# Performance work log

Hardware: AMD Instinct MI355X
Metric: run time of the kernel (lower is better)

The kernel has to match this reference:

```python
import jax, jax.numpy as jnp
import numpy as np

T, B, S, V = 50, 64, 400, 50000
D = 512; E = 512; H = 512; A = 512; POOL = 2


def setup_inputs() -> dict:
    key = jax.random.key(0)
    ks = jax.random.split(key, 20)
    def rn(k, shape, s=0.05):
        return jax.random.normal(k, shape, jnp.float32) * s
    return {
        "input_y": jax.random.randint(ks[0], (T, B), 0, V),
        "hidden": rn(ks[1], (1, B, H), 1.0),
        "context": rn(ks[2], (S, B, E), 1.0),
        "src_pad_mask": jnp.zeros((B, S), jnp.float32),
        "init_att": rn(ks[3], (B, E), 1.0),
        "coverage": jnp.zeros((B, S), jnp.float32),
        "global_ctx": rn(ks[4], (B, E), 1.0),
        "emb_W": rn(ks[5], (V, D)).at[0].set(0.0),  # padding_idx=0
        "W_ih": rn(ks[6], (3 * H, D + E)),
        "W_hh": rn(ks[7], (3 * H, H)),
        "b_ih": jnp.zeros((3 * H,), jnp.float32),
        "b_hh": jnp.zeros((3 * H,), jnp.float32),
        "W_pre": rn(ks[8], (E, A)),
        "b_pre": jnp.zeros((A,), jnp.float32),
        "W_q": rn(ks[9], (H + E, A)),
        "W_v": rn(ks[10], (A,)),
        "W_cov": rn(ks[11], (A,)),
        "W_pgen": rn(ks[12], (E + H + D,)),
        "b_pgen": jnp.zeros((), jnp.float32),
        "W_ro": rn(ks[13], (D + H + E + E, H)),
        "b_ro": jnp.zeros((H,), jnp.float32),
    }


def _gru_cell(x, h, W_ih, W_hh, b_ih, b_hh):
    # PyTorch GRUCell gate order: r, z, n
    gi = x @ W_ih.T + b_ih
    gh = h @ W_hh.T + b_hh
    i_r, i_z, i_n = jnp.split(gi, 3, axis=-1)
    h_r, h_z, h_n = jnp.split(gh, 3, axis=-1)
    r = jax.nn.sigmoid(i_r + h_r)
    z = jax.nn.sigmoid(i_z + h_z)
    n = jnp.tanh(i_n + r * h_n)
    return (1.0 - z) * n + z * h


def reference(input_y, hidden, context, src_pad_mask, init_att, coverage, global_ctx,
              emb_W, W_ih, W_hh, b_ih, b_hh, W_pre, b_pre, W_q, W_v, W_cov,
              W_pgen, b_pgen, W_ro, b_ro):
    emb = emb_W[input_y]                      # [T,B,D]
    ctx = jnp.transpose(context, (1, 0, 2))   # [B,S,E]
    precompute = ctx @ W_pre + b_pre          # [B,S,A] (computed once, as in module)
    pad = src_pad_mask > 0.5
    NEG = jnp.float32(-1e18)

    def step(carry, emb_t):
        h, cur_ctx, cov = carry
        x = jnp.concatenate([emb_t, cur_ctx], 1)          # input feed
        h0 = _gru_cell(x, h[0], W_ih, W_hh, b_ih, b_hh)   # layers=1
        h = h.at[0].set(h0)
        output = h0
        # concat attention with coverage
        q = jnp.concatenate([output, global_ctx], 1) @ W_q          # [B,A]
        tmp = jnp.tanh(precompute + q[:, None, :] + cov[..., None] * W_cov)
        energy = tmp @ W_v                                           # [B,S]
        energy = jnp.where(pad, NEG, energy)
        attn = jax.nn.softmax(energy, axis=1)
        cur_ctx = jnp.einsum('bs,bse->be', attn, ctx)
        # pointer-gen
        p_gen = jax.nn.sigmoid(
            jnp.concatenate([cur_ctx, output, emb_t], 1) @ W_pgen + b_pgen)[:, None]
        # readout + maxout (dropout is identity in eval)
        readout = jnp.concatenate([emb_t, output, cur_ctx, global_ctx], 1) @ W_ro + b_ro
        mo = readout.reshape(B, H // POOL, POOL).max(axis=-1)        # [B,H/POOL]
        cov_loss = jnp.sum(jnp.minimum(attn, cov), 1)                # cov_loss_wt=1.0
        next_cov = cov + attn
        return (h, cur_ctx, next_cov), (mo, p_gen, attn, cov_loss)

    (hidden_f, cur_ctx_f, cov_f), (g_out, g_pg, g_attn, cov_losses) = jax.lax.scan(
        step, (hidden, init_att, coverage), emb)
    return (g_out, hidden_f, g_attn[-1], cur_ctx_f, g_pg, g_attn, cov_losses, cov_f)
```

## Files before the change

### kernel.cpp

```cpp
#include <hip/hip_runtime.h>
#include <hip/hip_bf16.h>


#define T_STEPS 50
#define BB 64
#define SS 400

#define O_GOUT 0
#define O_HID 819200
#define O_ATTN_LAST 851968
#define O_CTXF 877568
#define O_PG 910336
#define O_GATTN 913536
#define O_COVL 2193536
#define O_COVF 2196736

typedef __attribute__((ext_vector_type(4))) float f4;
typedef __attribute__((ext_vector_type(8))) short s8v;
typedef __attribute__((ext_vector_type(4))) unsigned u4;

static __device__ __forceinline__ float bf2f(unsigned short u){
  unsigned v = ((unsigned)u) << 16; return __builtin_bit_cast(float, v);
}
static __device__ __forceinline__ unsigned short f2bf(float f){
  unsigned u = __builtin_bit_cast(unsigned, f);
  unsigned r = (u + 0x7FFFu + ((u >> 16) & 1u)) >> 16;
  return (unsigned short)r;
}
static __device__ __forceinline__ float sigmoidf_(float x){ return 1.f/(1.f+__expf(-x)); }
static __device__ __forceinline__ float tanhf_(float x){ float e=__expf(2.f*x); return 1.f - 2.f/(e+1.f); }
static __device__ __forceinline__ float ald32f(const float* p){
  unsigned u = __hip_atomic_load((const unsigned*)p, __ATOMIC_RELAXED, __HIP_MEMORY_SCOPE_AGENT);
  return __builtin_bit_cast(float, u);
}
static __device__ __forceinline__ void ast32f(float* p, float v){
  __hip_atomic_store((unsigned*)p, __builtin_bit_cast(unsigned, v),
                     __ATOMIC_RELAXED, __HIP_MEMORY_SCOPE_AGENT);
}

__global__ void conv_ctx(const float* __restrict__ ctx, unsigned short* __restrict__ out){
  int o = blockIdx.x*256 + threadIdx.x;
  if(o >= SS*BB*512) return;
  int e = o & 511; int b = (o>>9)&63; int s = o>>15;
  out[((b*SS+s)<<9) + e] = f2bf(ctx[o]);
}
__global__ void conv_emb(const int* __restrict__ y, const float* __restrict__ embW,
                         unsigned short* __restrict__ embU){
  int o = blockIdx.x*256+threadIdx.x; if(o>=T_STEPS*BB*512) return;
  int d = o & 511; int i = o>>9;
  embU[o] = f2bf(embW[(long)y[i]*512 + d]);
}
__global__ void conv_rest(const float* __restrict__ W_ih, const float* __restrict__ W_hh,
                          const float* __restrict__ W_pre, const float* __restrict__ W_ro,
                          const float* __restrict__ W_q,
                          const float* __restrict__ hidden, const float* __restrict__ init_att,
                          const float* __restrict__ gctx, const float* __restrict__ coverage,
                          unsigned short* __restrict__ wihbf, unsigned short* __restrict__ wpreT,
                          unsigned short* __restrict__ wroT, unsigned short* __restrict__ Wgru,
                          unsigned short* __restrict__ WqP,
                          float* __restrict__ hrow0, unsigned short* __restrict__ h0bf_init,
                          unsigned short* __restrict__ ctx0bf, float* __restrict__ gctxT,
                          float* __restrict__ cov, unsigned* __restrict__ flags){
  int o = blockIdx.x*256+threadIdx.x;
  if(o < 786432){
    int j = o>>9; int d = o&511;
    wihbf[o] = f2bf(W_ih[(long)j*1024 + d]);
  } else if(o < 1048576){
    int p = o - 786432;
    int a = p>>9; int e = p&511;
    wpreT[p] = f2bf(W_pre[(long)e*512 + a]);
  } else if(o < 2097152){
    int p = o - 1048576;
    int n = p>>11; int k = p&2047;
    wroT[p] = f2bf(W_ro[(long)k*512 + n]);
  } else if(o < 3670016){
    int p = o - 2097152;
    int rg = p >> 13; int rem = p & 8191;
    int ki = rem >> 9; int ln = (rem >> 3) & 63; int e = p & 7;
    int blk = rg/24; int r2 = rg%24; int w = r2/6; int r3 = r2%6; int g = r3>>1; int op = r3&1;
    int rl = ln & 15; int kk = ((ln>>4)<<3) + e;
    int d = blk*64 + w*16 + rl; int j = g*512 + d; int k = ki*32 + kk;
    float v = op ? W_hh[(long)j*512 + k] : W_ih[(long)j*1024 + 512 + k];
    Wgru[p] = f2bf(v);
  } else if(o < 3932160){
    int p = o - 3670016;
    int e = p&7; int ln=(p>>3)&63; int kf=(p>>9)&1; int nrg=(p>>10)&31; int blk=p>>15;
    int n = nrg*16 + (ln&15);
    int k = blk*64 + kf*32 + ((ln>>4)<<3) + e;
    WqP[p] = f2bf(W_q[(long)k*512 + n]);
  } else if(o < 4056128){
    int p = o - 3932160;
    if(p < 32768){ float v = hidden[p]; hrow0[p] = v; h0bf_init[p] = f2bf(v); }
    else if(p < 65536){ int q=p-32768; ctx0bf[q] = f2bf(init_att[q]); }
    else if(p < 98304){ int q=p-65536; int b=q>>9,e=q&511; gctxT[e*64+b]=gctx[q]; }
    else if(p < 123904){ int q=p-98304; cov[q]=coverage[q]; }
    else { int q=p-123904; if(q<64) flags[q]=0u; }
  }
}

template<int OUT_BF16>
__global__ __launch_bounds__(256) void mfma_gemm(
    const unsigned short* __restrict__ Abf, int lda,
    const unsigned short* __restrict__ Bbf, int ldb,
    void* __restrict__ Cp, int ldc, const float* __restrict__ bias, int K)
{
  __shared__ __align__(16) unsigned short Ash[128*40];
  __shared__ __align__(16) unsigned short Bsh[128*40];
  int m0 = blockIdx.x*128, n0 = blockIdx.y*128;
  int tid = threadIdx.x;
  int wid = tid>>6, lane = tid&63;
  int wm = wid>>1, wn = wid&1;
  int lr = lane&15, lg = lane>>4;
  f4 acc[4][4];
  #pragma unroll
  for(int i=0;i<4;i++)
    #pragma unroll
    for(int j=0;j<4;j++) acc[i][j]=(f4)0.f;

  for(int kt=0; kt<K; kt+=32){
    #pragma unroll
    for(int c=0;c<2;c++){
      int flat = tid*16 + c*8;
      int row = flat>>5, col = flat&31;
      const unsigned short* ga = Abf + (long)(m0+row)*lda + kt + col;
      *(uint4*)(&Ash[row*40+col]) = *(const uint4*)ga;
      const unsigned short* gb = Bbf + (long)(n0+row)*ldb + kt + col;
      *(uint4*)(&Bsh[row*40+col]) = *(const uint4*)gb;
    }
    __syncthreads();
    s8v av[4], bv[4];
    #pragma unroll
    for(int mi=0;mi<4;mi++) av[mi] = *(const s8v*)(&Ash[(wm*64+mi*16+lr)*40 + lg*8]);
    #pragma unroll
    for(int ni=0;ni<4;ni++) bv[ni] = *(const s8v*)(&Bsh[(wn*64+ni*16+lr)*40 + lg*8]);
    #pragma unroll
    for(int mi=0;mi<4;mi++)
      #pragma unroll
      for(int ni=0;ni<4;ni++)
        acc[mi][ni] = __builtin_amdgcn_mfma_f32_16x16x32_bf16(av[mi], bv[ni], acc[mi][ni], 0,0,0);
    __syncthreads();
  }
  #pragma unroll
  for(int mi=0;mi<4;mi++)
    #pragma unroll
    for(int ni=0;ni<4;ni++){
      int gc = n0 + wn*64 + ni*16 + lr;
      #pragma unroll
      for(int r=0;r<4;r++){
        int gr = m0 + wm*64 + mi*16 + lg*4 + r;
        float v = acc[mi][ni][r];
        if(bias) v += bias[gc];
        if(OUT_BF16) ((unsigned short*)Cp)[(long)gr*ldc + gc] = f2bf(v);
        else         ((float*)Cp)[(long)gr*ldc + gc] = v;
      }
    }
}

__global__ __launch_bounds__(256) void mfma_gemm_ro(
    const unsigned short* __restrict__ embU, const unsigned short* __restrict__ h0bf,
    const unsigned short* __restrict__ ctxA, const unsigned short* __restrict__ wroT,
    float* __restrict__ RO, const float* __restrict__ bias)
{
  __shared__ __align__(16) unsigned short Ash[128*40];
  __shared__ __align__(16) unsigned short Bsh[128*40];
  int m0 = blockIdx.x*128, n0 = blockIdx.y*128;
  int tid = threadIdx.x;
  int wid = tid>>6, lane = tid&63;
  int wm = wid>>1, wn = wid&1;
  int lr = lane&15, lg = lane>>4;
  f4 acc[4][4];
  #pragma unroll
  for(int i=0;i<4;i++)
    #pragma unroll
    for(int j=0;j<4;j++) acc[i][j]=(f4)0.f;

  for(int kt=0; kt<1536; kt+=32){
    const unsigned short* src = (kt<512) ? embU : (kt<1024) ? h0bf : ctxA;
    int klocal = kt & 511;
    #pragma unroll
    for(int c=0;c<2;c++){
      int flat = tid*16 + c*8;
      int row = flat>>5, col = flat&31;
      *(uint4*)(&Ash[row*40+col]) = *(const uint4*)(src + (long)(m0+row)*512 + klocal + col);
      *(uint4*)(&Bsh[row*40+col]) = *(const uint4*)(wroT + (long)(n0+row)*2048 + kt + col);
    }
    __syncthreads();
    s8v av[4], bv[4];
    #pragma unroll
    for(int mi=0;mi<4;mi++) av[mi] = *(const s8v*)(&Ash[(wm*64+mi*16+lr)*40 + lg*8]);
    #pragma unroll
    for(int ni=0;ni<4;ni++) bv[ni] = *(const s8v*)(&Bsh[(wn*64+ni*16+lr)*40 + lg*8]);
    #pragma unroll
    for(int mi=0;mi<4;mi++)
      #pragma unroll
      for(int ni=0;ni<4;ni++)
        acc[mi][ni] = __builtin_amdgcn_mfma_f32_16x16x32_bf16(av[mi], bv[ni], acc[mi][ni], 0,0,0);
    __syncthreads();
  }
  #pragma unroll
  for(int mi=0;mi<4;mi++)
    #pragma unroll
    for(int ni=0;ni<4;ni++){
      int gc = n0 + wn*64 + ni*16 + lr;
      #pragma unroll
      for(int r=0;r<4;r++){
        int gr = m0 + wm*64 + mi*16 + lg*4 + r;
        RO[(long)gr*512 + gc] = acc[mi][ni][r] + bias[gc];
      }
    }
}

__global__ __launch_bounds__(256) void small2(
  const float* __restrict__ AT, const float* __restrict__ W_q, const float* __restrict__ W_ro,
  float* __restrict__ q_g, float* __restrict__ ro_g)
{
  int blk = blockIdx.x;
  int half = blk>>7; int nblk = blk&127;
  int tid = threadIdx.x;
  int b = tid&63; int nq = tid>>6;
  int n = __builtin_amdgcn_readfirstlane(nblk*4 + nq);
  const float* W = half ? W_ro : W_q;
  int koff = half ? 1536 : 512;
  float acc = 0.f;
  const float* wp = W + (long)koff*512 + n;
  #pragma unroll 8
  for(int k=0;k<512;k++){
    acc = fmaf(AT[k*64+b], wp[(long)k*512], acc);
  }
  (half ? ro_g : q_g)[b*512+n] = acc;
}

__global__ __launch_bounds__(512) void k_step(
  const unsigned short* __restrict__ ctx0bf, float* __restrict__ ctxP,
  float* __restrict__ S_part, float* __restrict__ P_exp,
  const unsigned short* __restrict__ hprevbf,
  const float* __restrict__ hrow_in, float* __restrict__ hrow_out,
  const unsigned short* __restrict__ Wp, const unsigned short* __restrict__ WqP,
  const float* __restrict__ gi_emb, const float* __restrict__ b_hh,
  unsigned short* __restrict__ h0bf_all, float* __restrict__ qpart,
  float* __restrict__ cov, unsigned short* __restrict__ ctxA,
  const unsigned short* __restrict__ pre, const unsigned short* __restrict__ ctxbf,
  const float* __restrict__ q_g, const float* __restrict__ Wv,
  const float* __restrict__ Wcov, const float* __restrict__ padm,
  float* __restrict__ covl_part, unsigned* __restrict__ flags,
  float* __restrict__ outp, int t)
{
  __shared__ __align__(16) char smem[75008];
  const int blk = blockIdx.x;
  const int tid = threadIdx.x;
  const int w = tid>>6, lane = tid&63;
  const int lr = lane&15, lg = lane>>4;

  if(blk < 8){
    unsigned short* Ash = (unsigned short*)smem;
    unsigned short* HS  = (unsigned short*)(smem+65536);
    float* invS = (float*)(smem+74752);
    const int swz = (lr&7)<<4;
    const int dg = w&3, bh = w>>2;
    const int rgbase = blk*24 + dg*6;

    if(t>0 && tid<64){
      const float* Sp = S_part + ((t-1)&1)*256 + tid*4;
      invS[tid] = 1.f/(Sp[0]+Sp[1]+Sp[2]+Sp[3]);
    }
    __syncthreads();

    f4 acc2[6][2];
    #pragma unroll
    for(int u=0;u<6;u++)
      #pragma unroll
      for(int mm=0;mm<2;mm++) acc2[u][mm]=(f4)0.f;

    for(int kp=0; kp<2; kp++){
      for(int c = tid; c < 4096; c += 512){
        int op = c>>11; int row = (c>>5)&63; int kc = c&31;
        int e0 = kp*256 + kc*8;
        u4 v;
        if(op){
          v = *(const u4*)(hprevbf + row*512 + e0);
        } else if(t>0){
          const float* cp = ctxP + (long)row*2048 + e0;
          float sc = invS[row];
          f4 a0 = *(const f4*)(cp);
          f4 a1 = *(const f4*)(cp+512);
          f4 a2 = *(const f4*)(cp+1024);
          f4 a3 = *(const f4*)(cp+1536);
          f4 b0 = *(const f4*)(cp+4);
          f4 b1 = *(const f4*)(cp+516);
          f4 b2 = *(const f4*)(cp+1028);
          f4 b3 = *(const f4*)(cp+1540);
          f4 s0 = (a0+a1+a2+a3)*sc;
          f4 s1 = (b0+b1+b2+b3)*sc;
          v.x = (unsigned)f2bf(s0.x) | ((unsigned)f2bf(s0.y)<<16);
          v.y = (unsigned)f2bf(s0.z) | ((unsigned)f2bf(s0.w)<<16);
          v.z = (unsigned)f2bf(s1.x) | ((unsigned)f2bf(s1.y)<<16);
          v.w = (unsigned)f2bf(s1.z) | ((unsigned)f2bf(s1.w)<<16);
          if(blk == (row>>3))
            *(u4*)(ctxA + ((long)((t-1)*64+row))*512 + e0) = v;
        } else {
          v = *(const u4*)(ctx0bf + row*512 + e0);
        }
        int dst = op*32768 + row*512 + ((kc*16) ^ ((row&7)<<4));
        *(u4*)((char*)Ash + dst) = v;
      }
      __syncthreads();
      {
        #pragma unroll 2
        for(int ktl=0; ktl<256; ktl+=32){
          s8v av[2][2];
          #pragma unroll
          for(int op=0;op<2;op++)
            #pragma unroll
            for(int mm=0;mm<2;mm++){
              int mi = bh*2+mm;
              av[op][mm] = *(const s8v*)((const char*)Ash + op*32768 + (mi*16+lr)*512 + ((ktl*2 + lg*16) ^ swz));
            }
          int ki = kp*8 + (ktl>>5);
          const unsigned short* wb = Wp + (long)rgbase*8192 + ki*512 + lane*8;
          #pragma unroll
          for(int u=0;u<6;u++){
            s8v bv = *(const s8v*)(wb + (long)u*8192);
            #pragma unroll
            for(int mm=0;mm<2;mm++)
              acc2[u][mm] = __builtin_amdgcn_mfma_f32_16x16x32_bf16(av[u&1][mm], bv, acc2[u][mm], 0,0,0);
          }
        }
      }
      __syncthreads();
    }

    {
      int d = blk*64 + dg*16 + lr;
      float bhr = b_hh[d], bhz = b_hh[512+d], bhn = b_hh[1024+d];
      #pragma unroll
      for(int mm=0;mm<2;mm++){
        int mi = bh*2+mm;
        #pragma unroll
        for(int r=0;r<4;r++){
          int b = mi*16 + lg*4 + r;
          const float* ge = gi_emb + (long)(t*64+b)*1536;
          float g0 = __builtin_nontemporal_load(ge + d);
          float g1 = __builtin_nontemporal_load(ge + 512 + d);
          float g2 = __builtin_nontemporal_load(ge + 1024 + d);
          float rr = sigmoidf_(g0 + bhr + acc2[0][mm][r] + acc2[1][mm][r]);
          float zz = sigmoidf_(g1 + bhz + acc2[2][mm][r] + acc2[3][mm][r]);
          float nn = tanhf_(  g2       + acc2[4][mm][r] + rr*(acc2[5][mm][r] + bhn));
          float hp = hrow_in[b*512 + d];
          float hv = (1.f-zz)*nn + zz*hp;
          hrow_out[b*512+d] = hv;
          unsigned short hb = f2bf(hv);
          h0bf_all[(long)(t*64+b)*512 + d] = hb;
          HS[b*72 + dg*16 + lr] = hb;
          if(t==T_STEPS-1) outp[O_HID + b*512 + d] = hv;
        }
      }
    }
    __syncthreads();
    {
      #pragma unroll
      for(int i=0;i<8;i++){
        f4 accq[2];
        accq[0]=(f4)0.f; accq[1]=(f4)0.f;
        #pragma unroll
        for(int kf=0;kf<2;kf++){
          s8v bv = *(const s8v*)(WqP + ((((long)blk*32 + (dg*8+i))*2 + kf)*64 + lane)*8);
          #pragma unroll
          for(int mm=0;mm<2;mm++){
            int mi = bh*2+mm;
            s8v av = *(const s8v*)(HS + (mi*16+lr)*72 + kf*32 + lg*8);
            accq[mm] = __builtin_amdgcn_mfma_f32_16x16x32_bf16(av, bv, accq[mm], 0,0,0);
          }
        }
        int n = dg*128 + i*16 + lr;
        #pragma unroll
        for(int mm=0;mm<2;mm++)
          #pragma unroll
          for(int r=0;r<4;r++)
            ast32f(qpart + (long)blk*32768 + (long)((bh*2+mm)*16+lg*4+r)*512 + n, accq[mm][r]);
      }
    }
    asm volatile("s_waitcnt vmcnt(0)" ::: "memory");
    __syncthreads();
    if(tid==0)
      __hip_atomic_fetch_add(flags+t, 1u, __ATOMIC_RELEASE, __HIP_MEMORY_SCOPE_AGENT);
    return;
  }

  {
    int eb = blk-8; int b = eb>>2, cq = eb&3, c0 = cq*100;
    float* q_sh  = (float*)smem;
    float* wv_sh = (float*)(smem+2048);
    float* wc_sh = (float*)(smem+4096);
    float* covL  = (float*)(smem+6144);
    float* padL  = (float*)(smem+6560);
    float* red   = (float*)(smem+7392);
    float* red2  = (float*)(smem+9440);
    float* pb    = (float*)(smem+9472);

    wv_sh[tid]=Wv[tid]; wc_sh[tid]=Wcov[tid];
    if(tid<100) padL[tid]=padm[b*400+c0+tid];
    float clp = 0.f;
    if(t>0){
      const float* Sp = S_part + ((t-1)&1)*256 + b*4;
      float inv = 1.f/(Sp[0]+Sp[1]+Sp[2]+Sp[3]);
      if(tid<100){
        float p = P_exp[b*400+c0+tid]*inv;
        float co = cov[b*400+c0+tid];
        clp = fminf(p,co);
        float nc = co+p;
        cov[b*400+c0+tid]=nc;
        covL[tid]=nc;
        outp[O_GATTN + (long)(t-1)*25600 + b*400 + c0 + tid] = p;
      }
    } else {
      if(tid<100) covL[tid]=cov[b*400+c0+tid];
    }
    const unsigned short* prow = pre   + (((long)(b*400+c0))<<9) + lane*8;
    const unsigned short* crow = ctxbf + (((long)(b*400+c0))<<9) + lane*8;
    u4 pr[13], cr[13];
    #pragma unroll
    for(int j=0;j<13;j++){
      int i = w + j*8;
      long ro = (long)((i<100)? i : 0) << 9;
      pr[j] = *(const u4*)(prow + ro);
      cr[j] = *(const u4*)(crow + ro);
    }
    red[tid]=clp; __syncthreads();
    for(int o=256;o;o>>=1){ if(tid<o) red[tid]+=red[tid+o]; __syncthreads(); }
    if(t>0 && tid==0) covl_part[(long)(t-1)*256 + b*4+cq] = red[0];
    if(tid==0){
      unsigned it=0;
      while(__hip_atomic_load(flags+t, __ATOMIC_RELAXED, __HIP_MEMORY_SCOPE_AGENT) < 8u){
        __builtin_amdgcn_s_sleep(8);
        if(++it > 200000000u) break;
      }
    }
    __syncthreads();
    asm volatile("" ::: "memory");
    {
      float acc = q_g[b*512+tid];
      #pragma unroll
      for(int p=0;p<8;p++) acc += ald32f(qpart + ((long)p<<15) + b*512 + tid);
      q_sh[tid] = acc;
    }
    __syncthreads();
    float wsum = 0.f;
    float acc8[8];
    #pragma unroll
    for(int j=0;j<8;j++) acc8[j]=0.f;
    #pragma unroll
    for(int j=0;j<13;j++){
      int i = w + j*8;
      if(i<100){
        u4 cur = pr[j];
        const unsigned* uu = (const unsigned*)&cur;
        float cv = covL[i];
        float part = 0.f;
        #pragma unroll
        for(int q4=0;q4<4;q4++){
          int a = lane*8 + q4*2;
          part += wv_sh[a]  * tanhf_(bf2f((unsigned short)(uu[q4]&0xffffu)) + q_sh[a]   + cv*wc_sh[a]);
          part += wv_sh[a+1]* tanhf_(bf2f((unsigned short)(uu[q4]>>16))    + q_sh[a+1] + cv*wc_sh[a+1]);
        }
        #pragma unroll
        for(int off=32;off;off>>=1) part += __shfl_xor(part, off, 64);
        float e = (padL[i]>0.5f) ? -1e18f : part;
        float p = __expf(e);
        if(lane==0) P_exp[b*400+c0+i] = p;
        wsum += p;
        u4 cc = cr[j];
        const unsigned* cu = (const unsigned*)&cc;
        acc8[0] = fmaf(p, bf2f((unsigned short)(cu[0]&0xffffu)), acc8[0]);
        acc8[1] = fmaf(p, bf2f((unsigned short)(cu[0]>>16)),     acc8[1]);
        acc8[2] = fmaf(p, bf2f((unsigned short)(cu[1]&0xffffu)), acc8[2]);
        acc8[3] = fmaf(p, bf2f((unsigned short)(cu[1]>>16)),     acc8[3]);
        acc8[4] = fmaf(p, bf2f((unsigned short)(cu[2]&0xffffu)), acc8[4]);
        acc8[5] = fmaf(p, bf2f((unsigned short)(cu[2]>>16)),     acc8[5]);
        acc8[6] = fmaf(p, bf2f((unsigned short)(cu[3]&0xffffu)), acc8[6]);
        acc8[7] = fmaf(p, bf2f((unsigned short)(cu[3]>>16)),     acc8[7]);
      }
    }
    if(lane==0) red2[w]=wsum;
    __syncthreads();
    if(tid==0)
      S_part[(t&1)*256 + b*4+cq] = red2[0]+red2[1]+red2[2]+red2[3]+red2[4]+red2[5]+red2[6]+red2[7];
    #pragma unroll
    for(int j=0;j<8;j++) pb[w*512 + lane*8+j] = acc8[j];
    __syncthreads();
    {
      float v = pb[tid]+pb[512+tid]+pb[1024+tid]+pb[1536+tid]
               +pb[2048+tid]+pb[2560+tid]+pb[3072+tid]+pb[3584+tid];
      ctxP[((long)b*4+cq)*512 + tid] = v;
    }
  }
}

__global__ __launch_bounds__(256) void k_fin(
  const float* __restrict__ ctxP, const float* __restrict__ S_part,
  const float* __restrict__ P_exp, const float* __restrict__ cov,
  const float* __restrict__ covl_part,
  unsigned short* __restrict__ ctxA, float* __restrict__ outp)
{
  __shared__ float red[256];
  int b = blockIdx.x; int tid = threadIdx.x;
  const int tb = T_STEPS-1;
  const float* Sp = S_part + 256 + b*4;
  float S = Sp[0]+Sp[1]+Sp[2]+Sp[3];
  float inv = 1.f/S;
  float clp;
  {
    float p = P_exp[b*400+tid]*inv;
    float co = cov[b*400+tid];
    clp = fminf(p, co);
    float nc = co+p;
    outp[O_GATTN + (long)tb*25600 + b*400 + tid] = p;
    outp[O_ATTN_LAST + b*400 + tid] = p;
    outp[O_COVF + b*400 + tid] = nc;
  }
  if(tid<144){
    int i = 256+tid;
    float p = P_exp[b*400+i]*inv;
    float co = cov[b*400+i];
    clp += fminf(p, co);
    float nc = co+p;
    outp[O_GATTN + (long)tb*25600 + b*400 + i] = p;
    outp[O_ATTN_LAST + b*400 + i] = p;
    outp[O_COVF + b*400 + i] = nc;
  }
  red[tid]=clp; __syncthreads();
  for(int o=128;o;o>>=1){ if(tid<o) red[tid]+=red[tid+o]; __syncthreads(); }
  if(tid==0) outp[O_COVL + tb*64 + b] = red[0];
  if(tid<49){
    const float* cp = covl_part + (long)tid*256 + b*4;
    outp[O_COVL + tid*64 + b] = cp[0]+cp[1]+cp[2]+cp[3];
  }
  for(int c=tid;c<512;c+=256){
    float v = (ctxP[(long)b*2048+c]+ctxP[(long)b*2048+512+c]
              +ctxP[(long)b*2048+1024+c]+ctxP[(long)b*2048+1536+c])*inv;
    outp[O_CTXF + b*512 + c] = v;
    ctxA[(long)(tb*64+b)*512 + c] = f2bf(v);
  }
}

__global__ __launch_bounds__(256) void k_post(
  const unsigned short* __restrict__ embU, const unsigned short* __restrict__ h0bf,
  const unsigned short* __restrict__ ctxA, const float* __restrict__ Wpg,
  const float* __restrict__ bpg, const float* __restrict__ RO,
  const float* __restrict__ ro_g, float* __restrict__ outp)
{
  int blk = blockIdx.x;
  if(blk < 800){
    int wid = threadIdx.x>>6, lane=threadIdx.x&63;
    int m = blk*4 + wid;
    float acc=0.f;
    #pragma unroll
    for(int i=0;i<8;i++){
      int k = i*64+lane;
      acc = fmaf(bf2f(ctxA[(long)m*512+k]), Wpg[k], acc);
      acc = fmaf(bf2f(h0bf[(long)m*512+k]), Wpg[512+k], acc);
      acc = fmaf(bf2f(embU[(long)m*512+k]), Wpg[1024+k], acc);
    }
    #pragma unroll
    for(int off=32; off; off>>=1) acc += __shfl_xor(acc, off, 64);
    if(lane==0) outp[O_PG + m] = sigmoidf_(acc + bpg[0]);
  } else {
    int o = (blk-800)*256 + threadIdx.x;
    int h = o & 255; int m = o>>8; int b = m & 63;
    float v0 = RO[(long)m*512 + 2*h]   + ro_g[b*512 + 2*h];
    float v1 = RO[(long)m*512 + 2*h+1] + ro_g[b*512 + 2*h+1];
    outp[O_GOUT + o] = fmaxf(v0,v1);
  }
}

extern "C" void kernel_launch(void* const* d_in, const int* in_sizes, int n_in,
                              void* d_out, int out_size, void* d_ws, size_t ws_size,
                              hipStream_t stream)
{
  (void)in_sizes; (void)n_in; (void)out_size; (void)ws_size;
  const int*   y       = (const int*)d_in[0];
  const float* hidden  = (const float*)d_in[1];
  const float* context = (const float*)d_in[2];
  const float* padm    = (const float*)d_in[3];
  const float* init_att= (const float*)d_in[4];
  const float* coverage= (const float*)d_in[5];
  const float* gctx    = (const float*)d_in[6];
  const float* embW    = (const float*)d_in[7];
  const float* W_ih    = (const float*)d_in[8];
  const float* W_hh    = (const float*)d_in[9];
  const float* b_ih    = (const float*)d_in[10];
  const float* b_hh    = (const float*)d_in[11];
  const float* W_pre   = (const float*)d_in[12];
  const float* b_pre   = (const float*)d_in[13];
  const float* W_q     = (const float*)d_in[14];
  const float* W_v     = (const float*)d_in[15];
  const float* W_cov   = (const float*)d_in[16];
  const float* W_pg    = (const float*)d_in[17];
  const float* b_pg    = (const float*)d_in[18];
  const float* W_ro    = (const float*)d_in[19];
  const float* b_ro    = (const float*)d_in[20];
  float* out = (float*)d_out;

  char* wsb = (char*)d_ws;
  size_t off = 0;
  auto alloc = [&](size_t bytes)->char*{ char* p = wsb+off; off += (bytes+255)&~255UL; return p; };
  unsigned short* pre    = (unsigned short*)alloc(25600UL*512*2);
  unsigned short* ctxbf  = (unsigned short*)alloc(13107200UL*2);
  unsigned short* embU   = (unsigned short*)alloc(3200UL*512*2);
  unsigned short* wihbf  = (unsigned short*)alloc(1536UL*512*2);
  unsigned short* wpreT  = (unsigned short*)alloc(512UL*512*2);
  unsigned short* wroT   = (unsigned short*)alloc(512UL*2048*2);
  unsigned short* Wgru   = (unsigned short*)alloc(192UL*8192*2);
  unsigned short* WqP    = (unsigned short*)alloc(262144UL*2);
  float* gi_emb = (float*)alloc(3200UL*1536*4);
  float* RO     = (float*)alloc(3200UL*512*4);
  float* q_g    = (float*)alloc(64UL*512*4);
  float* ro_g   = (float*)alloc(64UL*512*4);
  float* hrow0  = (float*)alloc(64UL*512*4);
  float* hrow1  = (float*)alloc(64UL*512*4);
  float* gctxT  = (float*)alloc(512UL*64*4);
  unsigned short* h0bf = (unsigned short*)alloc(3200UL*512*2);
  unsigned short* h0bf_init = (unsigned short*)alloc(64UL*512*2);
  unsigned short* ctx0bf    = (unsigned short*)alloc(64UL*512*2);
  unsigned short* ctxA = (unsigned short*)alloc(3200UL*512*2);
  float* ctxP   = (float*)alloc(64UL*4*512*4);
  float* P_exp  = (float*)alloc(64UL*400*4);
  float* S_part = (float*)alloc(2UL*256*4);
  float* qpart  = (float*)alloc(8UL*64*512*4);
  float* cov    = (float*)alloc(64UL*400*4);
  float* covl_part = (float*)alloc(50UL*256*4);
  unsigned* flags = (unsigned*)alloc(64UL*4);

  conv_ctx <<<dim3(51200),dim3(256),0,stream>>>(context, ctxbf);
  conv_emb <<<dim3(6400), dim3(256),0,stream>>>(y, embW, embU);
  conv_rest<<<dim3(15845),dim3(256),0,stream>>>(W_ih, W_hh, W_pre, W_ro, W_q,
                                                hidden, init_att, gctx, coverage,
                                                wihbf, wpreT, wroT, Wgru, WqP,
                                                hrow0, h0bf_init, ctx0bf, gctxT, cov, flags);

  mfma_gemm<1><<<dim3(200,4),dim3(256),0,stream>>>(ctxbf,512, wpreT,512,  pre,   512, b_pre, 512);
  mfma_gemm<0><<<dim3(25,12),dim3(256),0,stream>>>(embU, 512, wihbf,512,  gi_emb,1536, b_ih, 512);
  small2<<<dim3(256),dim3(256),0,stream>>>(gctxT, W_q, W_ro, q_g, ro_g);

  for(int t=0; t<T_STEPS; t++){
    float* hin  = (t&1) ? hrow1 : hrow0;
    float* hout = (t&1) ? hrow0 : hrow1;
    const unsigned short* hprevbf = t ? (h0bf + (long)(t-1)*32768) : h0bf_init;
    k_step<<<dim3(264),dim3(512),0,stream>>>(ctx0bf, ctxP, S_part, P_exp, hprevbf,
                                             hin, hout, Wgru, WqP, gi_emb, b_hh,
                                             h0bf, qpart, cov, ctxA, pre, ctxbf,
                                             q_g, W_v, W_cov, padm, covl_part,
                                             flags, out, t);
  }

  k_fin<<<dim3(64),dim3(256),0,stream>>>(ctxP, S_part, P_exp, cov, covl_part, ctxA, out);
  mfma_gemm_ro<<<dim3(25,4),dim3(256),0,stream>>>(embU, h0bf, ctxA, wroT, RO, b_ro);
  k_post<<<dim3(4000),dim3(256),0,stream>>>(embU, h0bf, ctxA, W_pg, b_pg, RO, ro_g, out);
}
```

Before: 2.779 ms.

## Fuse per-step launches into one persistent cooperative scan kernel with flag sync

Replaces the 50 per-timestep k_step launches with one cooperative persistent kernel of 256 blocks that loops over time. GRU and attention blocks hand off through per-step atomic flags instead of kernel boundaries. The hidden state stays in registers, coverage stays in LDS, the attention block's own finalize runs in-kernel, and qpart is double-buffered. This removes launch overhead and the grid-wide barriers between steps. The cost is spin-wait latency and the correctness risk of a bounded spin loop that can break out early.

```diff
diff --git a/kernel.cpp b/kernel.cpp
--- a/kernel.cpp
+++ b/kernel.cpp
@@ -18,6 +18,7 @@
 typedef __attribute__((ext_vector_type(4))) float f4;
 typedef __attribute__((ext_vector_type(8))) short s8v;
 typedef __attribute__((ext_vector_type(4))) unsigned u4;
+typedef unsigned long long u64;
 
 static __device__ __forceinline__ float bf2f(unsigned short u){
   unsigned v = ((unsigned)u) << 16; return __builtin_bit_cast(float, v);
@@ -37,6 +38,14 @@
   __hip_atomic_store((unsigned*)p, __builtin_bit_cast(unsigned, v),
                      __ATOMIC_RELAXED, __HIP_MEMORY_SCOPE_AGENT);
 }
+static __device__ __forceinline__ u64 ald64(const void* p){
+  return __hip_atomic_load((const u64*)p, __ATOMIC_RELAXED, __HIP_MEMORY_SCOPE_AGENT);
+}
+static __device__ __forceinline__ void ast64(void* p, u64 v){
+  __hip_atomic_store((u64*)p, v, __ATOMIC_RELAXED, __HIP_MEMORY_SCOPE_AGENT);
+}
+static __device__ __forceinline__ float flo(u64 x){ return __builtin_bit_cast(float,(unsigned)x); }
+static __device__ __forceinline__ float fhi(u64 x){ return __builtin_bit_cast(float,(unsigned)(x>>32)); }
 
 __global__ void conv_ctx(const float* __restrict__ ctx, unsigned short* __restrict__ out){
   int o = blockIdx.x*256 + threadIdx.x;
@@ -58,7 +67,7 @@
                           unsigned short* __restrict__ wihbf, unsigned short* __restrict__ wpreT,
                           unsigned short* __restrict__ wroT, unsigned short* __restrict__ Wgru,
                           unsigned short* __restrict__ WqP,
-                          float* __restrict__ hrow0, unsigned short* __restrict__ h0bf_init,
+                          unsigned short* __restrict__ h0bf_init,
                           unsigned short* __restrict__ ctx0bf, float* __restrict__ gctxT,
                           float* __restrict__ cov, unsigned* __restrict__ flags){
   int o = blockIdx.x*256+threadIdx.x;
@@ -88,13 +97,13 @@
     int n = nrg*16 + (ln&15);
     int k = blk*64 + kf*32 + ((ln>>4)<<3) + e;
     WqP[p] = f2bf(W_q[(long)k*512 + n]);
-  } else if(o < 4056128){
+  } else if(o < 4060160){
     int p = o - 3932160;
-    if(p < 32768){ float v = hidden[p]; hrow0[p] = v; h0bf_init[p] = f2bf(v); }
+    if(p < 32768){ h0bf_init[p] = f2bf(hidden[p]); }
     else if(p < 65536){ int q=p-32768; ctx0bf[q] = f2bf(init_att[q]); }
     else if(p < 98304){ int q=p-65536; int b=q>>9,e=q&511; gctxT[e*64+b]=gctx[q]; }
     else if(p < 123904){ int q=p-98304; cov[q]=coverage[q]; }
-    else { int q=p-123904; if(q<64) flags[q]=0u; }
+    else { int q=p-123904; flags[q]=0u; }
   }
 }
 
@@ -230,81 +239,245 @@
   (half ? ro_g : q_g)[b*512+n] = acc;
 }
 
-__global__ __launch_bounds__(512) void k_step(
+#define L_ASH   0
+#define L_HS    65536
+#define L_INVS  74752
+#define L_QSH   75008
+#define L_WVS   77056
+#define L_WCS   79104
+#define L_COVL  81152
+#define L_PADL  81568
+#define L_PL    81984
+#define L_RED   82400
+#define L_RED2  84448
+#define L_SS    84480
+#define L_PB    84496
+#define L_TOTAL 100896
+
+#define SPIN_BOUND 400000u
+
+__global__ __launch_bounds__(512, 2) void k_scan(
   const unsigned short* __restrict__ ctx0bf, float* __restrict__ ctxP,
   float* __restrict__ S_part, float* __restrict__ P_exp,
-  const unsigned short* __restrict__ hprevbf,
-  const float* __restrict__ hrow_in, float* __restrict__ hrow_out,
+  const unsigned short* __restrict__ h0bf_init, const float* __restrict__ hidden,
   const unsigned short* __restrict__ Wp, const unsigned short* __restrict__ WqP,
   const float* __restrict__ gi_emb, const float* __restrict__ b_hh,
   unsigned short* __restrict__ h0bf_all, float* __restrict__ qpart,
   float* __restrict__ cov, unsigned short* __restrict__ ctxA,
+  unsigned short* __restrict__ hX,
   const unsigned short* __restrict__ pre, const unsigned short* __restrict__ ctxbf,
   const float* __restrict__ q_g, const float* __restrict__ Wv,
   const float* __restrict__ Wcov, const float* __restrict__ padm,
   float* __restrict__ covl_part, unsigned* __restrict__ flags,
-  float* __restrict__ outp, int t)
+  float* __restrict__ outp)
 {
-  __shared__ __align__(16) char smem[75008];
+  __shared__ __align__(16) char smem[L_TOTAL];
   const int blk = blockIdx.x;
   const int tid = threadIdx.x;
   const int w = tid>>6, lane = tid&63;
   const int lr = lane&15, lg = lane>>4;
+  const int b = blk>>2, cq = blk&3, c0 = cq*100;
+
+  float* q_sh  = (float*)(smem+L_QSH);
+  float* wv_sh = (float*)(smem+L_WVS);
+  float* wc_sh = (float*)(smem+L_WCS);
+  float* covL  = (float*)(smem+L_COVL);
+  float* padL  = (float*)(smem+L_PADL);
+  float* pL    = (float*)(smem+L_PL);
+  float* red   = (float*)(smem+L_RED);
+  float* red2  = (float*)(smem+L_RED2);
+  float* sS    = (float*)(smem+L_SS);
+  float* pb    = (float*)(smem+L_PB);
+
+  wv_sh[tid]=Wv[tid]; wc_sh[tid]=Wcov[tid];
+  if(tid<100){ padL[tid]=padm[b*400+c0+tid]; covL[tid]=cov[b*400+c0+tid]; }
+  __syncthreads();
+
+  const unsigned short* prow = pre   + (((long)(b*400+c0))<<9) + lane*8;
+  const unsigned short* crow = ctxbf + (((long)(b*400+c0))<<9) + lane*8;
+
+#define WAIT_OWN_FLAG_E(tt) \
+  if(tid==0){ unsigned it=0; \
+    while(__hip_atomic_load(&flags[128+(tt)*64+b], __ATOMIC_RELAXED, __HIP_MEMORY_SCOPE_AGENT) < 4u){ \
+      __builtin_amdgcn_s_sleep(4); if(++it>SPIN_BOUND) break; } } \
+  __syncthreads(); asm volatile("" ::: "memory");
+
+#define CALC_INVS(tt) \
+  if(tid==0){ const float* Sp = S_part + ((tt)&1)*256 + b*4; \
+    sS[0] = 1.f/(ald32f(Sp)+ald32f(Sp+1)+ald32f(Sp+2)+ald32f(Sp+3)); } \
+  __syncthreads();
+
+#define FINALIZE(tt) { \
+  float invSv = sS[0]; \
+  float clp = 0.f; \
+  if(tid<100){ \
+    float p = pL[tid]*invSv; \
+    float co = covL[tid]; \
+    clp = fminf(p,co); \
+    covL[tid] = co+p; \
+    outp[O_GATTN + (long)(tt)*25600 + b*400 + c0 + tid] = p; \
+  } \
+  red[tid]=clp; __syncthreads(); \
+  for(int o=256;o;o>>=1){ if(tid<o) red[tid]+=red[tid+o]; __syncthreads(); } \
+  if(tid==0) covl_part[(long)(tt)*256 + b*4+cq] = red[0]; \
+  __syncthreads(); }
+
+#define WAIT_FLAG_G(tt) \
+  if(tid==0){ unsigned it=0; \
+    while(__hip_atomic_load(&flags[64+(tt)], __ATOMIC_RELAXED, __HIP_MEMORY_SCOPE_AGENT) < 8u){ \
+      __builtin_amdgcn_s_sleep(4); if(++it>SPIN_BOUND) break; } } \
+  __syncthreads(); asm volatile("" ::: "memory");
+
+#define Q_REDUCE(tt) { \
+  const float* qp = qpart + ((tt)&1)*262144; \
+  float acc = q_g[b*512+tid]; \
+  _Pragma("unroll") \
+  for(int p=0;p<8;p++) acc += ald32f(qp + ((long)p<<15) + b*512 + tid); \
+  q_sh[tid] = acc; } \
+  __syncthreads();
+
+#define ENERGY_BODY(tt, PRJ, CRJ) { \
+  float wsum = 0.f; \
+  float acc8[8]; \
+  _Pragma("unroll") for(int j8=0;j8<8;j8++) acc8[j8]=0.f; \
+  _Pragma("unroll") \
+  for(int j=0;j<13;j++){ \
+    int i = w + j*8; \
+    if(i<100){ \
+      u4 cur = (PRJ); \
+      const unsigned* uu = (const unsigned*)&cur; \
+      float cv = covL[i]; \
+      float part = 0.f; \
+      _Pragma("unroll") \
+      for(int q4=0;q4<4;q4++){ \
+        int a = lane*8 + q4*2; \
+        part += wv_sh[a]  * tanhf_(bf2f((unsigned short)(uu[q4]&0xffffu)) + q_sh[a]   + cv*wc_sh[a]); \
+        part += wv_sh[a+1]* tanhf_(bf2f((unsigned short)(uu[q4]>>16))    + q_sh[a+1] + cv*wc_sh[a+1]); \
+      } \
+      _Pragma("unroll") \
+      for(int off=32;off;off>>=1) part += __shfl_xor(part, off, 64); \
+      float e = (padL[i]>0.5f) ? -1e18f : part; \
+      float p = __expf(e); \
+      if(lane==0){ pL[i] = p; P_exp[b*400+c0+i] = p; } \
+      wsum += p; \
+      u4 cc = (CRJ); \
+      const unsigned* cu = (const unsigned*)&cc; \
+      acc8[0] = fmaf(p, bf2f((unsigned short)(cu[0]&0xffffu)), acc8[0]); \
+      acc8[1] = fmaf(p, bf2f((unsigned short)(cu[0]>>16)),     acc8[1]); \
+      acc8[2] = fmaf(p, bf2f((unsigned short)(cu[1]&0xffffu)), acc8[2]); \
+      acc8[3] = fmaf(p, bf2f((unsigned short)(cu[1]>>16)),     acc8[3]); \
+      acc8[4] = fmaf(p, bf2f((unsigned short)(cu[2]&0xffffu)), acc8[4]); \
+      acc8[5] = fmaf(p, bf2f((unsigned short)(cu[2]>>16)),     acc8[5]); \
+      acc8[6] = fmaf(p, bf2f((unsigned short)(cu[3]&0xffffu)), acc8[6]); \
+      acc8[7] = fmaf(p, bf2f((unsigned short)(cu[3]>>16)),     acc8[7]); \
+    } \
+  } \
+  if(lane==0) red2[w]=wsum; \
+  __syncthreads(); \
+  if(tid==0){ \
+    float s = red2[0]+red2[1]+red2[2]+red2[3]+red2[4]+red2[5]+red2[6]+red2[7]; \
+    ast32f(S_part + ((tt)&1)*256 + b*4+cq, s); \
+  } \
+  _Pragma("unroll") for(int j8=0;j8<8;j8++) pb[w*512 + lane*8+j8] = acc8[j8]; \
+  __syncthreads(); \
+  { \
+    float v = pb[tid]+pb[512+tid]+pb[1024+tid]+pb[1536+tid] \
+             +pb[2048+tid]+pb[2560+tid]+pb[3072+tid]+pb[3584+tid]; \
+    ast32f(ctxP + ((long)b*4+cq)*512 + tid, v); \
+  } \
+  asm volatile("s_waitcnt vmcnt(0)" ::: "memory"); \
+  __syncthreads(); \
+  if(tid==0) \
+    __hip_atomic_fetch_add(&flags[128 + (tt)*64 + b], 1u, __ATOMIC_RELEASE, __HIP_MEMORY_SCOPE_AGENT); \
+  __syncthreads(); }
 
   if(blk < 8){
-    unsigned short* Ash = (unsigned short*)smem;
-    unsigned short* HS  = (unsigned short*)(smem+65536);
-    float* invS = (float*)(smem+74752);
+    unsigned short* Ash = (unsigned short*)(smem+L_ASH);
+    unsigned short* HS  = (unsigned short*)(smem+L_HS);
+    float* invS = (float*)(smem+L_INVS);
+    const int gblk = blk;
     const int swz = (lr&7)<<4;
     const int dg = w&3, bh = w>>2;
-    const int rgbase = blk*24 + dg*6;
-
-    if(t>0 && tid<64){
-      const float* Sp = S_part + ((t-1)&1)*256 + tid*4;
-      invS[tid] = 1.f/(Sp[0]+Sp[1]+Sp[2]+Sp[3]);
-    }
-    __syncthreads();
-
-    f4 acc2[6][2];
-    #pragma unroll
-    for(int u=0;u<6;u++)
+    const int rgbase = gblk*24 + dg*6;
+
+    float h_reg[2][2][4];
+    {
+      int d = gblk*64 + dg*16 + lr;
       #pragma unroll
-      for(int mm=0;mm<2;mm++) acc2[u][mm]=(f4)0.f;
-
-    for(int kp=0; kp<2; kp++){
-      for(int c = tid; c < 4096; c += 512){
-        int op = c>>11; int row = (c>>5)&63; int kc = c&31;
-        int e0 = kp*256 + kc*8;
-        u4 v;
-        if(op){
-          v = *(const u4*)(hprevbf + row*512 + e0);
-        } else if(t>0){
-          const float* cp = ctxP + (long)row*2048 + e0;
-          float sc = invS[row];
-          f4 a0 = *(const f4*)(cp);
-          f4 a1 = *(const f4*)(cp+512);
-          f4 a2 = *(const f4*)(cp+1024);
-          f4 a3 = *(const f4*)(cp+1536);
-          f4 b0 = *(const f4*)(cp+4);
-          f4 b1 = *(const f4*)(cp+516);
-          f4 b2 = *(const f4*)(cp+1028);
-          f4 b3 = *(const f4*)(cp+1540);
-          f4 s0 = (a0+a1+a2+a3)*sc;
-          f4 s1 = (b0+b1+b2+b3)*sc;
-          v.x = (unsigned)f2bf(s0.x) | ((unsigned)f2bf(s0.y)<<16);
-          v.y = (unsigned)f2bf(s0.z) | ((unsigned)f2bf(s0.w)<<16);
-          v.z = (unsigned)f2bf(s1.x) | ((unsigned)f2bf(s1.y)<<16);
-          v.w = (unsigned)f2bf(s1.z) | ((unsigned)f2bf(s1.w)<<16);
-          if(blk == (row>>3))
-            *(u4*)(ctxA + ((long)((t-1)*64+row))*512 + e0) = v;
-        } else {
-          v = *(const u4*)(ctx0bf + row*512 + e0);
+      for(int mm=0;mm<2;mm++)
+        #pragma unroll
+        for(int r=0;r<4;r++)
+          h_reg[0][mm][r] = hidden[(long)(((bh*2+mm)*16+lg*4+r))*512 + d];
+    }
+
+    #pragma unroll 1
+    for(int t=0;t<T_STEPS;t++){
+      if(t>0){
+        if(w==0){
+          unsigned it=0;
+          for(;;){
+            unsigned vv = __hip_atomic_load(&flags[128+(t-1)*64+lane], __ATOMIC_RELAXED, __HIP_MEMORY_SCOPE_AGENT);
+            if(__all(vv>=4u)) break;
+            __builtin_amdgcn_s_sleep(4);
+            if(++it>SPIN_BOUND) break;
+          }
         }
-        int dst = op*32768 + row*512 + ((kc*16) ^ ((row&7)<<4));
-        *(u4*)((char*)Ash + dst) = v;
+        __syncthreads(); asm volatile("" ::: "memory");
+        CALC_INVS(t-1)
+        FINALIZE(t-1)
+        if(tid<64){
+          const float* Sp = S_part + ((t-1)&1)*256 + tid*4;
+          invS[tid] = 1.f/(ald32f(Sp)+ald32f(Sp+1)+ald32f(Sp+2)+ald32f(Sp+3));
+        }
+        __syncthreads();
       }
-      __syncthreads();
-      {
+
+      const unsigned short* hXr = hX + ((t-1)&1)*32768;
+      unsigned short* hXw = hX + (t&1)*32768;
+      f4 acc2[6][2];
+      #pragma unroll
+      for(int u=0;u<6;u++){ acc2[u][0]=(f4)0.f; acc2[u][1]=(f4)0.f; }
+
+      for(int kp=0; kp<2; kp++){
+        for(int c = tid; c < 4096; c += 512){
+          int op = c>>11; int row = (c>>5)&63; int kc = c&31;
+          int e0 = kp*256 + kc*8;
+          u4 v;
+          if(op){
+            if(t>0){
+              const unsigned short* hs = hXr + row*512 + e0;
+              u64 lo = ald64(hs), hi2 = ald64(hs+4);
+              v.x=(unsigned)lo; v.y=(unsigned)(lo>>32); v.z=(unsigned)hi2; v.w=(unsigned)(hi2>>32);
+            } else {
+              v = *(const u4*)(h0bf_init + row*512 + e0);
+            }
+          } else {
+            if(t>0){
+              const float* cp = ctxP + (long)row*2048 + e0;
+              float sc = invS[row];
+              float s0=0,s1=0,s2=0,s3=0,s4=0,s5=0,s6=0,s7=0;
+              #pragma unroll
+              for(int p4=0;p4<4;p4++){
+                const float* pp = cp + p4*512;
+                u64 a0=ald64(pp), a1=ald64(pp+2), a2=ald64(pp+4), a3=ald64(pp+6);
+                s0+=flo(a0); s1+=fhi(a0); s2+=flo(a1); s3+=fhi(a1);
+                s4+=flo(a2); s5+=fhi(a2); s6+=flo(a3); s7+=fhi(a3);
+              }
+              s0*=sc; s1*=sc; s2*=sc; s3*=sc; s4*=sc; s5*=sc; s6*=sc; s7*=sc;
+              v.x = (unsigned)f2bf(s0) | ((unsigned)f2bf(s1)<<16);
+              v.y = (unsigned)f2bf(s2) | ((unsigned)f2bf(s3)<<16);
+              v.z = (unsigned)f2bf(s4) | ((unsigned)f2bf(s5)<<16);
+              v.w = (unsigned)f2bf(s6) | ((unsigned)f2bf(s7)<<16);
+              if(gblk == (row>>3))
+                *(u4*)(ctxA + ((long)((t-1)*64+row))*512 + e0) = v;
+            } else {
+              v = *(const u4*)(ctx0bf + row*512 + e0);
+            }
+          }
+          int dst = op*32768 + row*512 + ((kc*16) ^ ((row&7)<<4));
+          *(u4*)((char*)Ash + dst) = v;
+        }
+        __syncthreads();
         #pragma unroll 2
         for(int ktl=0; ktl<256; ktl+=32){
           s8v av[2][2];
@@ -325,98 +498,79 @@
               acc2[u][mm] = __builtin_amdgcn_mfma_f32_16x16x32_bf16(av[u&1][mm], bv, acc2[u][mm], 0,0,0);
           }
         }
+        __syncthreads();
+      }
+      {
+        int d = gblk*64 + dg*16 + lr;
+        float bhr = b_hh[d], bhz = b_hh[512+d], bhn = b_hh[1024+d];
+        #pragma unroll
+        for(int mm=0;mm<2;mm++){
+          #pragma unroll
+          for(int r=0;r<4;r++){
+            int bb = (bh*2+mm)*16 + lg*4 + r;
+            const float* ge = gi_emb + (long)(t*64+bb)*1536;
+            float g0 = __builtin_nontemporal_load(ge + d);
+            float g1 = __builtin_nontemporal_load(ge + 512 + d);
+            float g2 = __builtin_nontemporal_load(ge + 1024 + d);
+            float rr = sigmoidf_(g0 + bhr + acc2[0][mm][r] + acc2[1][mm][r]);
+            float zz = sigmoidf_(g1 + bhz + acc2[2][mm][r] + acc2[3][mm][r]);
+            float nn = tanhf_(  g2       + acc2[4][mm][r] + rr*(acc2[5][mm][r] + bhn));
+            float hv = (1.f-zz)*nn + zz*h_reg[0][mm][r];
+            h_reg[0][mm][r] = hv;
+            unsigned short hb = f2bf(hv);
+            h0bf_all[(long)(t*64+bb)*512 + d] = hb;
+            HS[bb*72 + dg*16 + lr] = hb;
+            if(t==T_STEPS-1) outp[O_HID + bb*512 + d] = hv;
+          }
+        }
       }
       __syncthreads();
-    }
-
-    {
-      int d = blk*64 + dg*16 + lr;
-      float bhr = b_hh[d], bhz = b_hh[512+d], bhn = b_hh[1024+d];
-      #pragma unroll
-      for(int mm=0;mm<2;mm++){
-        int mi = bh*2+mm;
+      for(int c=tid;c<1024;c+=512){
+        int bb=c>>4, d8=c&15;
+        u64 v = *(const u64*)(HS + bb*72 + d8*4);
+        ast64(hXw + bb*512 + gblk*64 + d8*4, v);
+      }
+      {
+        float* qp = qpart + (t&1)*262144;
         #pragma unroll
-        for(int r=0;r<4;r++){
-          int b = mi*16 + lg*4 + r;
-          const float* ge = gi_emb + (long)(t*64+b)*1536;
-          float g0 = __builtin_nontemporal_load(ge + d);
-          float g1 = __builtin_nontemporal_load(ge + 512 + d);
-          float g2 = __builtin_nontemporal_load(ge + 1024 + d);
-          float rr = sigmoidf_(g0 + bhr + acc2[0][mm][r] + acc2[1][mm][r]);
-          float zz = sigmoidf_(g1 + bhz + acc2[2][mm][r] + acc2[3][mm][r]);
-          float nn = tanhf_(  g2       + acc2[4][mm][r] + rr*(acc2[5][mm][r] + bhn));
-          float hp = hrow_in[b*512 + d];
-          float hv = (1.f-zz)*nn + zz*hp;
-          hrow_out[b*512+d] = hv;
-          unsigned short hb = f2bf(hv);
-          h0bf_all[(long)(t*64+b)*512 + d] = hb;
-          HS[b*72 + dg*16 + lr] = hb;
-          if(t==T_STEPS-1) outp[O_HID + b*512 + d] = hv;
+        for(int i=0;i<8;i++){
+          f4 accq[2];
+          accq[0]=(f4)0.f; accq[1]=(f4)0.f;
+          #pragma unroll
+          for(int kf=0;kf<2;kf++){
+            s8v bv = *(const s8v*)(WqP + ((((long)gblk*32 + (dg*8+i))*2 + kf)*64 + lane)*8);
+            #pragma unroll
+            for(int mm=0;mm<2;mm++){
+              int mi = bh*2+mm;
+              s8v av = *(const s8v*)(HS + (mi*16+lr)*72 + kf*32 + lg*8);
+              accq[mm] = __builtin_amdgcn_mfma_f32_16x16x32_bf16(av, bv, accq[mm], 0,0,0);
+            }
+          }
+          int n = dg*128 + i*16 + lr;
+          #pragma unroll
+          for(int mm=0;mm<2;mm++)
+            #pragma unroll
+            for(int r=0;r<4;r++)
+              ast32f(qp + (long)gblk*32768 + (long)((bh*2+mm)*16+lg*4+r)*512 + n, accq[mm][r]);
         }
       }
+      asm volatile("s_waitcnt vmcnt(0)" ::: "memory");
+      __syncthreads();
+      if(tid==0)
+        __hip_atomic_fetch_add(&flags[64+t], 1u, __ATOMIC_RELEASE, __HIP_MEMORY_SCOPE_AGENT);
+
+      WAIT_FLAG_G(t)
+      Q_REDUCE(t)
+      ENERGY_BODY(t,
+        (*(const u4*)(prow + ((long)i<<9))),
+        (*(const u4*)(crow + ((long)i<<9))))
     }
     __syncthreads();
-    {
-      #pragma unroll
-      for(int i=0;i<8;i++){
-        f4 accq[2];
-        accq[0]=(f4)0.f; accq[1]=(f4)0.f;
-        #pragma unroll
-        for(int kf=0;kf<2;kf++){
-          s8v bv = *(const s8v*)(WqP + ((((long)blk*32 + (dg*8+i))*2 + kf)*64 + lane)*8);
-          #pragma unroll
-          for(int mm=0;mm<2;mm++){
-            int mi = bh*2+mm;
-            s8v av = *(const s8v*)(HS + (mi*16+lr)*72 + kf*32 + lg*8);
-            accq[mm] = __builtin_amdgcn_mfma_f32_16x16x32_bf16(av, bv, accq[mm], 0,0,0);
-          }
-        }
-        int n = dg*128 + i*16 + lr;
-        #pragma unroll
-        for(int mm=0;mm<2;mm++)
-          #pragma unroll
-          for(int r=0;r<4;r++)
-            ast32f(qpart + (long)blk*32768 + (long)((bh*2+mm)*16+lg*4+r)*512 + n, accq[mm][r]);
-      }
-    }
-    asm volatile("s_waitcnt vmcnt(0)" ::: "memory");
-    __syncthreads();
-    if(tid==0)
-      __hip_atomic_fetch_add(flags+t, 1u, __ATOMIC_RELEASE, __HIP_MEMORY_SCOPE_AGENT);
+    if(tid<100) cov[b*400+c0+tid] = covL[tid];
     return;
   }
 
   {
-    int eb = blk-8; int b = eb>>2, cq = eb&3, c0 = cq*100;
-    float* q_sh  = (float*)smem;
-    float* wv_sh = (float*)(smem+2048);
-    float* wc_sh = (float*)(smem+4096);
-    float* covL  = (float*)(smem+6144);
-    float* padL  = (float*)(smem+6560);
-    float* red   = (float*)(smem+7392);
-    float* red2  = (float*)(smem+9440);
-    float* pb    = (float*)(smem+9472);
-
-    wv_sh[tid]=Wv[tid]; wc_sh[tid]=Wcov[tid];
-    if(tid<100) padL[tid]=padm[b*400+c0+tid];
-    float clp = 0.f;
-    if(t>0){
-      const float* Sp = S_part + ((t-1)&1)*256 + b*4;
-      float inv = 1.f/(Sp[0]+Sp[1]+Sp[2]+Sp[3]);
-      if(tid<100){
-        float p = P_exp[b*400+c0+tid]*inv;
-        float co = cov[b*400+c0+tid];
-        clp = fminf(p,co);
-        float nc = co+p;
-        cov[b*400+c0+tid]=nc;
-        covL[tid]=nc;
-        outp[O_GATTN + (long)(t-1)*25600 + b*400 + c0 + tid] = p;
-      }
-    } else {
-      if(tid<100) covL[tid]=cov[b*400+c0+tid];
-    }
-    const unsigned short* prow = pre   + (((long)(b*400+c0))<<9) + lane*8;
-    const unsigned short* crow = ctxbf + (((long)(b*400+c0))<<9) + lane*8;
     u4 pr[13], cr[13];
     #pragma unroll
     for(int j=0;j<13;j++){
@@ -425,73 +579,19 @@
       pr[j] = *(const u4*)(prow + ro);
       cr[j] = *(const u4*)(crow + ro);
     }
-    red[tid]=clp; __syncthreads();
-    for(int o=256;o;o>>=1){ if(tid<o) red[tid]+=red[tid+o]; __syncthreads(); }
-    if(t>0 && tid==0) covl_part[(long)(t-1)*256 + b*4+cq] = red[0];
-    if(tid==0){
-      unsigned it=0;
-      while(__hip_atomic_load(flags+t, __ATOMIC_RELAXED, __HIP_MEMORY_SCOPE_AGENT) < 8u){
-        __builtin_amdgcn_s_sleep(8);
-        if(++it > 200000000u) break;
+    #pragma unroll 1
+    for(int t=0;t<T_STEPS;t++){
+      if(t>0){
+        WAIT_OWN_FLAG_E(t-1)
+        CALC_INVS(t-1)
+        FINALIZE(t-1)
       }
+      WAIT_FLAG_G(t)
+      Q_REDUCE(t)
+      ENERGY_BODY(t, pr[j], cr[j])
     }
     __syncthreads();
-    asm volatile("" ::: "memory");
-    {
-      float acc = q_g[b*512+tid];
-      #pragma unroll
-      for(int p=0;p<8;p++) acc += ald32f(qpart + ((long)p<<15) + b*512 + tid);
-      q_sh[tid] = acc;
-    }
-    __syncthreads();
-    float wsum = 0.f;
-    float acc8[8];
-    #pragma unroll
-    for(int j=0;j<8;j++) acc8[j]=0.f;
-    #pragma unroll
-    for(int j=0;j<13;j++){
-      int i = w + j*8;
-      if(i<100){
-        u4 cur = pr[j];
-        const unsigned* uu = (const unsigned*)&cur;
-        float cv = covL[i];
-        float part = 0.f;
-        #pragma unroll
-        for(int q4=0;q4<4;q4++){
-          int a = lane*8 + q4*2;
-          part += wv_sh[a]  * tanhf_(bf2f((unsigned short)(uu[q4]&0xffffu)) + q_sh[a]   + cv*wc_sh[a]);
-          part += wv_sh[a+1]* tanhf_(bf2f((unsigned short)(uu[q4]>>16))    + q_sh[a+1] + cv*wc_sh[a+1]);
-        }
-        #pragma unroll
-        for(int off=32;off;off>>=1) part += __shfl_xor(part, off, 64);
-        float e = (padL[i]>0.5f) ? -1e18f : part;
-        float p = __expf(e);
-        if(lane==0) P_exp[b*400+c0+i] = p;
-        wsum += p;
-        u4 cc = cr[j];
-        const unsigned* cu = (const unsigned*)&cc;
-        acc8[0] = fmaf(p, bf2f((unsigned short)(cu[0]&0xffffu)), acc8[0]);
-        acc8[1] = fmaf(p, bf2f((unsigned short)(cu[0]>>16)),     acc8[1]);
-        acc8[2] = fmaf(p, bf2f((unsigned short)(cu[1]&0xffffu)), acc8[2]);
-        acc8[3] = fmaf(p, bf2f((unsigned short)(cu[1]>>16)),     acc8[3]);
-        acc8[4] = fmaf(p, bf2f((unsigned short)(cu[2]&0xffffu)), acc8[4]);
-        acc8[5] = fmaf(p, bf2f((unsigned short)(cu[2]>>16)),     acc8[5]);
-        acc8[6] = fmaf(p, bf2f((unsigned short)(cu[3]&0xffffu)), acc8[6]);
-        acc8[7] = fmaf(p, bf2f((unsigned short)(cu[3]>>16)),     acc8[7]);
-      }
-    }
-    if(lane==0) red2[w]=wsum;
-    __syncthreads();
-    if(tid==0)
-      S_part[(t&1)*256 + b*4+cq] = red2[0]+red2[1]+red2[2]+red2[3]+red2[4]+red2[5]+red2[6]+red2[7];
-    #pragma unroll
-    for(int j=0;j<8;j++) pb[w*512 + lane*8+j] = acc8[j];
-    __syncthreads();
-    {
-      float v = pb[tid]+pb[512+tid]+pb[1024+tid]+pb[1536+tid]
-               +pb[2048+tid]+pb[2560+tid]+pb[3072+tid]+pb[3584+tid];
-      ctxP[((long)b*4+cq)*512 + tid] = v;
-    }
+    if(tid<100) cov[b*400+c0+tid] = covL[tid];
   }
 }
 
@@ -615,41 +715,51 @@
   float* RO     = (float*)alloc(3200UL*512*4);
   float* q_g    = (float*)alloc(64UL*512*4);
   float* ro_g   = (float*)alloc(64UL*512*4);
-  float* hrow0  = (float*)alloc(64UL*512*4);
-  float* hrow1  = (float*)alloc(64UL*512*4);
   float* gctxT  = (float*)alloc(512UL*64*4);
   unsigned short* h0bf = (unsigned short*)alloc(3200UL*512*2);
   unsigned short* h0bf_init = (unsigned short*)alloc(64UL*512*2);
   unsigned short* ctx0bf    = (unsigned short*)alloc(64UL*512*2);
   unsigned short* ctxA = (unsigned short*)alloc(3200UL*512*2);
+  unsigned short* hX   = (unsigned short*)alloc(2UL*32768*2);
   float* ctxP   = (float*)alloc(64UL*4*512*4);
   float* P_exp  = (float*)alloc(64UL*400*4);
   float* S_part = (float*)alloc(2UL*256*4);
-  float* qpart  = (float*)alloc(8UL*64*512*4);
+  float* qpart  = (float*)alloc(2UL*262144*4);
   float* cov    = (float*)alloc(64UL*400*4);
   float* covl_part = (float*)alloc(50UL*256*4);
-  unsigned* flags = (unsigned*)alloc(64UL*4);
+  unsigned* flags = (unsigned*)alloc(4096UL*4);
 
   conv_ctx <<<dim3(51200),dim3(256),0,stream>>>(context, ctxbf);
   conv_emb <<<dim3(6400), dim3(256),0,stream>>>(y, embW, embU);
-  conv_rest<<<dim3(15845),dim3(256),0,stream>>>(W_ih, W_hh, W_pre, W_ro, W_q,
+  conv_rest<<<dim3(15860),dim3(256),0,stream>>>(W_ih, W_hh, W_pre, W_ro, W_q,
                                                 hidden, init_att, gctx, coverage,
                                                 wihbf, wpreT, wroT, Wgru, WqP,
-                                                hrow0, h0bf_init, ctx0bf, gctxT, cov, flags);
+                                                h0bf_init, ctx0bf, gctxT, cov, flags);
 
   mfma_gemm<1><<<dim3(200,4),dim3(256),0,stream>>>(ctxbf,512, wpreT,512,  pre,   512, b_pre, 512);
   mfma_gemm<0><<<dim3(25,12),dim3(256),0,stream>>>(embU, 512, wihbf,512,  gi_emb,1536, b_ih, 512);
   small2<<<dim3(256),dim3(256),0,stream>>>(gctxT, W_q, W_ro, q_g, ro_g);
 
-  for(int t=0; t<T_STEPS; t++){
-    float* hin  = (t&1) ? hrow1 : hrow0;
-    float* hout = (t&1) ? hrow0 : hrow1;
-    const unsigned short* hprevbf = t ? (h0bf + (long)(t-1)*32768) : h0bf_init;
-    k_step<<<dim3(264),dim3(512),0,stream>>>(ctx0bf, ctxP, S_part, P_exp, hprevbf,
-                                             hin, hout, Wgru, WqP, gi_emb, b_hh,
-                                             h0bf, qpart, cov, ctxA, pre, ctxbf,
-                                             q_g, W_v, W_cov, padm, covl_part,
-                                             flags, out, t);
+  {
+    const unsigned short *ctx0_c=ctx0bf, *h0i_c=h0bf_init, *wp_c=Wgru, *wqp_c=WqP,
+                         *pre_c=pre, *ctxbf_c=ctxbf;
+    float *ctxP_p=ctxP, *S_p=S_part, *Pe_p=P_exp, *qp_p=qpart, *cov_p=cov,
+          *covl_p=covl_part, *out_p=out;
+    unsigned short *h0bf_p=h0bf, *ctxA_p=ctxA, *hX_p=hX;
+    unsigned* fl_p=flags;
+    const float *hid_c=hidden, *gi_c=gi_emb, *bhh_c=b_hh, *qg_c=q_g,
+                *wv_c=W_v, *wcov_c=W_cov, *padm_c=padm;
+    void* args[] = {
+      (void*)&ctx0_c, (void*)&ctxP_p, (void*)&S_p, (void*)&Pe_p,
+      (void*)&h0i_c, (void*)&hid_c, (void*)&wp_c, (void*)&wqp_c,
+      (void*)&gi_c, (void*)&bhh_c, (void*)&h0bf_p, (void*)&qp_p,
+      (void*)&cov_p, (void*)&ctxA_p, (void*)&hX_p,
+      (void*)&pre_c, (void*)&ctxbf_c, (void*)&qg_c, (void*)&wv_c,
+      (void*)&wcov_c, (void*)&padm_c, (void*)&covl_p, (void*)&fl_p,
+      (void*)&out_p
+    };
+    hipLaunchCooperativeKernel(reinterpret_cast<void*>(k_scan),
+                               dim3(256), dim3(512), args, 0, stream);
   }
 
   k_fin<<<dim3(64),dim3(256),0,stream>>>(ctxP, S_part, P_exp, cov, covl_part, ctxA, out);
```

Result: slower. 4.968 ms (+78.8%).
